# Kernel optimization log

Hardware: AMD Instinct MI355X
Metric: run time of the kernel (lower is better)

The kernel has to match this reference:

```python
import jax, jax.numpy as jnp
import numpy as np

FP8_MAX = 448.0  # e4m3fn max


def _fake_quant_fp8(x, scale):
    # quantize: scale, clamp, round-trip through float8_e4m3fn; dequantize by 1/scale
    xq = jnp.clip(x * scale, -FP8_MAX, FP8_MAX).astype(jnp.float8_e4m3fn)
    return xq.astype(jnp.float32) * (1.0 / scale)


def _compute_scale(x):
    amax = jnp.max(jnp.abs(x))
    return FP8_MAX / jnp.maximum(amax, 1e-12)


def setup_inputs() -> dict:
    key = jax.random.key(0)
    kx, kw = jax.random.split(key)
    x = jax.random.normal(kx, (8, 2048, 4096), dtype=jnp.float32)
    weight = jax.random.normal(kw, (4096, 4096), dtype=jnp.float32) * 0.02
    return {"x": x, "weight": weight}


def reference(x, weight):
    B, S, K = x.shape
    N = weight.shape[1]
    # weight path: per-tensor scale, fp8 round-trip (transpose in original is value-preserving)
    w_dq = _fake_quant_fp8(weight, _compute_scale(weight))  # [K, N]
    # activation path
    x2d = x.reshape(-1, K)  # [M, K]
    x_dq = _fake_quant_fp8(x2d, _compute_scale(x2d))
    out = x_dq @ w_dq  # fp32 GEMM, [M, N]
    return out.reshape(B, S, N)
```

## Files before the change

kernel.cpp:

```cpp
#include <hip/hip_runtime.h>
#include <stdint.h>

#define FP8_MAX 448.0f

typedef float f32x4 __attribute__((ext_vector_type(4)));
typedef int i32x8 __attribute__((ext_vector_type(8)));
typedef int i32x4 __attribute__((ext_vector_type(4)));

__device__ __forceinline__ unsigned int pack4_fp8(float4 v, float s) {
  float a = fminf(fmaxf(v.x * s, -FP8_MAX), FP8_MAX);
  float b = fminf(fmaxf(v.y * s, -FP8_MAX), FP8_MAX);
  float c = fminf(fmaxf(v.z * s, -FP8_MAX), FP8_MAX);
  float d = fminf(fmaxf(v.w * s, -FP8_MAX), FP8_MAX);
  unsigned int r = (unsigned int)__builtin_amdgcn_cvt_pk_fp8_f32(a, b, 0, false);
  r = (unsigned int)__builtin_amdgcn_cvt_pk_fp8_f32(c, d, (int)r, true);
  return r;
}

__device__ __forceinline__ void load16_to_lds(const void* g, void* l) {
  auto gp = (const __attribute__((address_space(1))) void*)(uintptr_t)g;
  auto lp = (__attribute__((address_space(3))) void*)(unsigned int)(uintptr_t)l;
  __builtin_amdgcn_global_load_lds(gp, lp, 16, 0, 0);
}

__global__ void amax_kernel(const float* __restrict__ p, int n4, unsigned int* __restrict__ slot) {
  int i = blockIdx.x * blockDim.x + threadIdx.x;
  int stride = gridDim.x * blockDim.x;
  float m = 0.0f;
  const float4* p4 = (const float4*)p;
  for (; i < n4; i += stride) {
    float4 v = p4[i];
    m = fmaxf(m, fmaxf(fmaxf(fabsf(v.x), fabsf(v.y)), fmaxf(fabsf(v.z), fabsf(v.w))));
  }
#pragma unroll
  for (int off = 32; off > 0; off >>= 1)
    m = fmaxf(m, __shfl_down(m, off, 64));
  __shared__ float wmax[4];
  int lane = threadIdx.x & 63;
  int wv = threadIdx.x >> 6;
  if (lane == 0) wmax[wv] = m;
  __syncthreads();
  if (threadIdx.x == 0) {
    m = fmaxf(fmaxf(wmax[0], wmax[1]), fmaxf(wmax[2], wmax[3]));
    atomicMax(slot, __float_as_uint(m));
  }
}

__global__ void quant_x_kernel(const float* __restrict__ x, unsigned int* __restrict__ xq,
                               const unsigned int* __restrict__ hdr, int n4) {
  float s = FP8_MAX / fmaxf(__uint_as_float(hdr[0]), 1e-12f);
  int i = blockIdx.x * blockDim.x + threadIdx.x;
  int stride = gridDim.x * blockDim.x;
  const float4* x4 = (const float4*)x;
  for (; i < n4; i += stride)
    xq[i] = pack4_fp8(x4[i], s);
}

__global__ void quant_w_t_kernel(const float* __restrict__ w, unsigned char* __restrict__ wqT,
                                 const unsigned int* __restrict__ hdr, int K, int N) {
  __shared__ unsigned int tileT[64][17];
  float s = FP8_MAX / fmaxf(__uint_as_float(hdr[1]), 1e-12f);
  int tk0 = blockIdx.y << 6;
  int tn0 = blockIdx.x << 6;
  int t = threadIdx.x;

  int rn = (t & 15) << 2;
  int rk = (t >> 4) << 2;
  unsigned int wrow[4];
#pragma unroll
  for (int j = 0; j < 4; ++j) {
    float4 v = *(const float4*)(w + (size_t)(tk0 + rk + j) * N + tn0 + rn);
    wrow[j] = pack4_fp8(v, s);
  }
#pragma unroll
  for (int i = 0; i < 4; ++i) {
    unsigned int colw = ((wrow[0] >> (8 * i)) & 0xffu)
                      | (((wrow[1] >> (8 * i)) & 0xffu) << 8)
                      | (((wrow[2] >> (8 * i)) & 0xffu) << 16)
                      | (((wrow[3] >> (8 * i)) & 0xffu) << 24);
    tileT[rn + i][rk >> 2] = colw;
  }
  __syncthreads();

  int n = t >> 2;
  int kc = (t & 3) << 2;
  uint4 v = make_uint4(tileT[n][kc], tileT[n][kc + 1], tileT[n][kc + 2], tileT[n][kc + 3]);
  *(uint4*)(wqT + (size_t)(tn0 + n) * K + tk0 + (kc << 2)) = v;
}

__global__ __launch_bounds__(256, 2) void gemm_fp8_kernel(
    const unsigned char* __restrict__ Aq,
    const unsigned char* __restrict__ Bq,
    const unsigned int* __restrict__ hdr,
    float* __restrict__ out, int M, int N, int K) {
  __shared__ __align__(16) unsigned char As[128 * 128];
  __shared__ __align__(16) unsigned char Bs[128 * 128];

  const int t = threadIdx.x;
  const int wave = t >> 6;
  const int lane = t & 63;
  const int row16 = lane & 15;
  const int quad = lane >> 4;
  const int m0 = blockIdx.y << 7;
  const int n0 = blockIdx.x << 7;
  const int waveM = (wave >> 1) << 6;
  const int waveN = (wave & 1) << 6;

  const int rowS = (wave << 3) + (lane >> 3);
  const int colS = (((lane & 7) ^ ((lane >> 3) & 7)) << 4);

  const unsigned char* ag = Aq + (size_t)(m0 + rowS) * K + colS;
  const unsigned char* bg = Bq + (size_t)(n0 + rowS) * K + colS;
  unsigned char* al = &As[rowS * 128 + ((lane & 7) << 4)];
  unsigned char* bl = &Bs[rowS * 128 + ((lane & 7) << 4)];
  const size_t gStep = (size_t)32 * K;

  const int sw = row16 & 7;
  const int off0 = (((quad << 1) ^ sw) << 4);

  f32x4 acc[4][4] = {};

  for (int k0 = 0; k0 < K; k0 += 128) {
#pragma unroll
    for (int j = 0; j < 4; ++j)
      load16_to_lds(ag + k0 + j * gStep, al + j * 4096);
#pragma unroll
    for (int j = 0; j < 4; ++j)
      load16_to_lds(bg + k0 + j * gStep, bl + j * 4096);
    __syncthreads();

    i32x8 af[4], bf[4];
#pragma unroll
    for (int mi = 0; mi < 4; ++mi) {
      const unsigned char* p = As + (waveM + mi * 16 + row16) * 128;
      i32x4 lo = *(const i32x4*)(p + off0);
      i32x4 hi = *(const i32x4*)(p + (off0 ^ 16));
      af[mi] = __builtin_shufflevector(lo, hi, 0, 1, 2, 3, 4, 5, 6, 7);
    }
#pragma unroll
    for (int ni = 0; ni < 4; ++ni) {
      const unsigned char* p = Bs + (waveN + ni * 16 + row16) * 128;
      i32x4 lo = *(const i32x4*)(p + off0);
      i32x4 hi = *(const i32x4*)(p + (off0 ^ 16));
      bf[ni] = __builtin_shufflevector(lo, hi, 0, 1, 2, 3, 4, 5, 6, 7);
    }
#pragma unroll
    for (int mi = 0; mi < 4; ++mi)
#pragma unroll
      for (int ni = 0; ni < 4; ++ni)
        acc[mi][ni] = __builtin_amdgcn_mfma_scale_f32_16x16x128_f8f6f4(
            af[mi], bf[ni], acc[mi][ni],
            0 , 0 ,
            0, 0x7f7f7f7f ,
            0, 0x7f7f7f7f );
    __syncthreads();
  }

  const float ax = fmaxf(__uint_as_float(hdr[0]), 1e-12f);
  const float aw = fmaxf(__uint_as_float(hdr[1]), 1e-12f);
  const float sc = (ax / FP8_MAX) * (aw / FP8_MAX);
#pragma unroll
  for (int mi = 0; mi < 4; ++mi) {
#pragma unroll
    for (int ni = 0; ni < 4; ++ni) {
      const int gc = n0 + waveN + ni * 16 + row16;
#pragma unroll
      for (int r = 0; r < 4; ++r) {
        const int gr = m0 + waveM + mi * 16 + quad * 4 + r;
        out[(size_t)gr * N + gc] = acc[mi][ni][r] * sc;
      }
    }
  }
}

extern "C" void kernel_launch(void* const* d_in, const int* in_sizes, int n_in,
                              void* d_out, int out_size, void* d_ws, size_t ws_size,
                              hipStream_t stream) {
  const float* x = (const float*)d_in[0];
  const float* w = (const float*)d_in[1];
  float* out = (float*)d_out;

  const int K = 4096;
  const int N = 4096;
  const int M = in_sizes[0] / K;

  unsigned int* hdr = (unsigned int*)d_ws;
  unsigned char* xq = (unsigned char*)d_ws + 16;
  unsigned char* wqT = xq + (size_t)M * K;

  hipMemsetAsync(d_ws, 0, 16, stream);

  amax_kernel<<<2048, 256, 0, stream>>>(x, (int)((size_t)M * K / 4), hdr + 0);
  amax_kernel<<<1024, 256, 0, stream>>>(w, (int)((size_t)K * N / 4), hdr + 1);

  quant_x_kernel<<<4096, 256, 0, stream>>>(x, (unsigned int*)xq, hdr, (int)((size_t)M * K / 4));
  quant_w_t_kernel<<<dim3(N / 64, K / 64), 256, 0, stream>>>(w, wqT, hdr, K, N);

  gemm_fp8_kernel<<<dim3(N / 128, M / 128), 256, 0, stream>>>(xq, wqT, hdr, out, M, N, K);
}
```

Baseline: 886.8 us.

## Use 256x256 double-buffered pipelined FP8 GEMM and fuse amax kernels

The FP8 GEMM moves from 128x128 tiles with 256 threads to 256x256 tiles with 512 threads and a 128 KB double-buffered LDS. Global-to-LDS loads for the next tiles are interleaved with MFMA quarters, using explicit vmcnt/lgkmcnt waits, barriers and s_setprio. The goal is to hide load latency and raise data reuse per block. The two amax reductions are also merged into a single launch. The costs are higher LDS use, which leaves one block per CU, and hand-placed waits that must stay correct as the pipeline runs down.

```diff
diff --git a/kernel.cpp b/kernel.cpp
--- a/kernel.cpp
+++ b/kernel.cpp
@@ -23,11 +23,20 @@
   __builtin_amdgcn_global_load_lds(gp, lp, 16, 0, 0);
 }
 
-__global__ void amax_kernel(const float* __restrict__ p, int n4, unsigned int* __restrict__ slot) {
-  int i = blockIdx.x * blockDim.x + threadIdx.x;
-  int stride = gridDim.x * blockDim.x;
+__global__ void amax2_kernel(const float* __restrict__ x, int n4x,
+                             const float* __restrict__ w, int n4w,
+                             unsigned int* __restrict__ hdr) {
+  const float4* p4;
+  int n4, base, nblk;
+  unsigned int* slot;
+  if (blockIdx.x < 2048) {
+    p4 = (const float4*)x; n4 = n4x; base = blockIdx.x; nblk = 2048; slot = hdr;
+  } else {
+    p4 = (const float4*)w; n4 = n4w; base = blockIdx.x - 2048; nblk = 512; slot = hdr + 1;
+  }
+  int i = base * blockDim.x + threadIdx.x;
+  int stride = nblk * blockDim.x;
   float m = 0.0f;
-  const float4* p4 = (const float4*)p;
   for (; i < n4; i += stride) {
     float4 v = p4[i];
     m = fmaxf(m, fmaxf(fmaxf(fabsf(v.x), fabsf(v.y)), fmaxf(fabsf(v.z), fabsf(v.w))));
@@ -88,85 +97,150 @@
   *(uint4*)(wqT + (size_t)(tn0 + n) * K + tk0 + (kc << 2)) = v;
 }
 
-__global__ __launch_bounds__(256, 2) void gemm_fp8_kernel(
+__device__ __forceinline__ i32x8 read_frag(const unsigned char* p, int off0) {
+  i32x4 lo = *(const i32x4*)(p + off0);
+  i32x4 hi = *(const i32x4*)(p + (off0 ^ 16));
+  return __builtin_shufflevector(lo, hi, 0, 1, 2, 3, 4, 5, 6, 7);
+}
+
+#define MFMA1(a, b, c) \
+  __builtin_amdgcn_mfma_scale_f32_16x16x128_f8f6f4(a, b, c, 0, 0, 0, 0x7f7f7f7f, 0, 0x7f7f7f7f)
+
+#define MFMA_Q(M0_, N0_)                                              \
+  do {                                                                \
+    __builtin_amdgcn_s_setprio(1);                                    \
+    acc[M0_ + 0][N0_ + 0] = MFMA1(af[0], bf[N0_ + 0], acc[M0_ + 0][N0_ + 0]); \
+    acc[M0_ + 0][N0_ + 1] = MFMA1(af[0], bf[N0_ + 1], acc[M0_ + 0][N0_ + 1]); \
+    acc[M0_ + 1][N0_ + 0] = MFMA1(af[1], bf[N0_ + 0], acc[M0_ + 1][N0_ + 0]); \
+    acc[M0_ + 1][N0_ + 1] = MFMA1(af[1], bf[N0_ + 1], acc[M0_ + 1][N0_ + 1]); \
+    acc[M0_ + 2][N0_ + 0] = MFMA1(af[2], bf[N0_ + 0], acc[M0_ + 2][N0_ + 0]); \
+    acc[M0_ + 2][N0_ + 1] = MFMA1(af[2], bf[N0_ + 1], acc[M0_ + 2][N0_ + 1]); \
+    acc[M0_ + 3][N0_ + 0] = MFMA1(af[3], bf[N0_ + 0], acc[M0_ + 3][N0_ + 0]); \
+    acc[M0_ + 3][N0_ + 1] = MFMA1(af[3], bf[N0_ + 1], acc[M0_ + 3][N0_ + 1]); \
+    __builtin_amdgcn_s_setprio(0);                                    \
+  } while (0)
+
+#define BAR() __builtin_amdgcn_s_barrier()
+#define LGKM0()                                           \
+  do {                                                    \
+    asm volatile("s_waitcnt lgkmcnt(0)" ::: "memory");    \
+    __builtin_amdgcn_sched_barrier(0);                    \
+  } while (0)
+#define VMCNT(N_)                                               \
+  do {                                                          \
+    asm volatile("s_waitcnt vmcnt(" #N_ ")" ::: "memory");      \
+    __builtin_amdgcn_sched_barrier(0);                          \
+  } while (0)
+
+__global__ __launch_bounds__(512, 2) void gemm_fp8_kernel(
     const unsigned char* __restrict__ Aq,
     const unsigned char* __restrict__ Bq,
     const unsigned int* __restrict__ hdr,
     float* __restrict__ out, int M, int N, int K) {
-  __shared__ __align__(16) unsigned char As[128 * 128];
-  __shared__ __align__(16) unsigned char Bs[128 * 128];
+  __shared__ __align__(16) unsigned char smem[131072];
 
   const int t = threadIdx.x;
   const int wave = t >> 6;
   const int lane = t & 63;
   const int row16 = lane & 15;
   const int quad = lane >> 4;
-  const int m0 = blockIdx.y << 7;
-  const int n0 = blockIdx.x << 7;
-  const int waveM = (wave >> 1) << 6;
-  const int waveN = (wave & 1) << 6;
-
-  const int rowS = (wave << 3) + (lane >> 3);
-  const int colS = (((lane & 7) ^ ((lane >> 3) & 7)) << 4);
-
-  const unsigned char* ag = Aq + (size_t)(m0 + rowS) * K + colS;
-  const unsigned char* bg = Bq + (size_t)(n0 + rowS) * K + colS;
-  unsigned char* al = &As[rowS * 128 + ((lane & 7) << 4)];
-  unsigned char* bl = &Bs[rowS * 128 + ((lane & 7) << 4)];
-  const size_t gStep = (size_t)32 * K;
-
-  const int sw = row16 & 7;
-  const int off0 = (((quad << 1) ^ sw) << 4);
-
-  f32x4 acc[4][4] = {};
-
-  for (int k0 = 0; k0 < K; k0 += 128) {
-#pragma unroll
-    for (int j = 0; j < 4; ++j)
-      load16_to_lds(ag + k0 + j * gStep, al + j * 4096);
-#pragma unroll
-    for (int j = 0; j < 4; ++j)
-      load16_to_lds(bg + k0 + j * gStep, bl + j * 4096);
-    __syncthreads();
-
+  const int wr = wave >> 2;
+  const int wc = wave & 3;
+  const int m0 = blockIdx.y << 8;
+  const int n0 = blockIdx.x << 8;
+
+  const int sRow = (wave << 3) + (lane >> 3);
+  const int sCol = (((lane & 7) ^ (lane >> 3)) << 4);
+  const unsigned char* agBase = Aq + (size_t)(m0 + sRow) * K + sCol;
+  const unsigned char* bgBase = Bq + (size_t)(n0 + sRow) * K + sCol;
+  const int ldsStageOff = (wave << 10) + (lane << 4);
+
+  auto stageA = [&](int u, int h) {
+    const int buf = (u & 1) << 15;
+#pragma unroll
+    for (int r = 0; r < 2; ++r)
+      load16_to_lds(agBase + (size_t)((h << 7) + (r << 6)) * K + ((size_t)u << 7),
+                    smem + buf + (h << 14) + (r << 13) + ldsStageOff);
+  };
+  auto stageB = [&](int u, int h) {
+    const int buf = (u & 1) << 15;
+#pragma unroll
+    for (int r = 0; r < 2; ++r)
+      load16_to_lds(bgBase + (size_t)((h << 7) + (r << 6)) * K + ((size_t)u << 7),
+                    smem + 65536 + buf + (h << 14) + (r << 13) + ldsStageOff);
+  };
+
+  const int off0 = (((quad << 1) ^ (row16 & 7)) << 4);
+  const int aRow = (wr << 7) + row16;
+  const int bRow = (wc << 6) + row16;
+
+  f32x4 acc[8][4] = {};
+
+  const int NT = K >> 7;
+
+  stageA(0, 0); stageA(0, 1); stageB(0, 0); stageB(0, 1);
+  stageA(1, 0); stageB(1, 0);
+  VMCNT(4);
+  BAR();
+
+  auto tile_body = [&](int tt, bool stg1, bool stg2, int waitN) {
+    const int buf = (tt & 1) << 15;
+    const unsigned char* Ab = smem + buf;
+    const unsigned char* Bb = smem + 65536 + buf;
     i32x8 af[4], bf[4];
-#pragma unroll
-    for (int mi = 0; mi < 4; ++mi) {
-      const unsigned char* p = As + (waveM + mi * 16 + row16) * 128;
-      i32x4 lo = *(const i32x4*)(p + off0);
-      i32x4 hi = *(const i32x4*)(p + (off0 ^ 16));
-      af[mi] = __builtin_shufflevector(lo, hi, 0, 1, 2, 3, 4, 5, 6, 7);
+    af[0] = read_frag(Ab + ((aRow + 0) << 7), off0);
+    af[1] = read_frag(Ab + ((aRow + 16) << 7), off0);
+    af[2] = read_frag(Ab + ((aRow + 32) << 7), off0);
+    af[3] = read_frag(Ab + ((aRow + 48) << 7), off0);
+    bf[0] = read_frag(Bb + ((bRow + 0) << 7), off0);
+    bf[1] = read_frag(Bb + ((bRow + 16) << 7), off0);
+    if (stg1) stageA(tt + 1, 1);
+    BAR();
+    LGKM0();
+    MFMA_Q(0, 0);
+    BAR();
+    bf[2] = read_frag(Bb + ((bRow + 32) << 7), off0);
+    bf[3] = read_frag(Bb + ((bRow + 48) << 7), off0);
+    if (stg1) stageB(tt + 1, 1);
+    BAR();
+    LGKM0();
+    MFMA_Q(0, 2);
+    BAR();
+    af[0] = read_frag(Ab + ((aRow + 64) << 7), off0);
+    af[1] = read_frag(Ab + ((aRow + 80) << 7), off0);
+    af[2] = read_frag(Ab + ((aRow + 96) << 7), off0);
+    af[3] = read_frag(Ab + ((aRow + 112) << 7), off0);
+    if (stg2) stageB(tt + 2, 0);
+    BAR();
+    LGKM0();
+    MFMA_Q(4, 0);
+    BAR();
+    if (stg2) stageA(tt + 2, 0);
+    if (waitN == 4) {
+      VMCNT(4);
+    } else if (waitN == 0) {
+      VMCNT(0);
     }
-#pragma unroll
-    for (int ni = 0; ni < 4; ++ni) {
-      const unsigned char* p = Bs + (waveN + ni * 16 + row16) * 128;
-      i32x4 lo = *(const i32x4*)(p + off0);
-      i32x4 hi = *(const i32x4*)(p + (off0 ^ 16));
-      bf[ni] = __builtin_shufflevector(lo, hi, 0, 1, 2, 3, 4, 5, 6, 7);
-    }
-#pragma unroll
-    for (int mi = 0; mi < 4; ++mi)
-#pragma unroll
-      for (int ni = 0; ni < 4; ++ni)
-        acc[mi][ni] = __builtin_amdgcn_mfma_scale_f32_16x16x128_f8f6f4(
-            af[mi], bf[ni], acc[mi][ni],
-            0 , 0 ,
-            0, 0x7f7f7f7f ,
-            0, 0x7f7f7f7f );
-    __syncthreads();
-  }
+    BAR();
+    MFMA_Q(4, 2);
+    BAR();
+  };
+
+  for (int tt = 0; tt < NT - 2; ++tt) tile_body(tt, true, true, 4);
+  tile_body(NT - 2, true, false, 0);
+  tile_body(NT - 1, false, false, -1);
 
   const float ax = fmaxf(__uint_as_float(hdr[0]), 1e-12f);
   const float aw = fmaxf(__uint_as_float(hdr[1]), 1e-12f);
   const float sc = (ax / FP8_MAX) * (aw / FP8_MAX);
 #pragma unroll
-  for (int mi = 0; mi < 4; ++mi) {
+  for (int mi = 0; mi < 8; ++mi) {
 #pragma unroll
     for (int ni = 0; ni < 4; ++ni) {
-      const int gc = n0 + waveN + ni * 16 + row16;
+      const int gc = n0 + (wc << 6) + ni * 16 + row16;
 #pragma unroll
       for (int r = 0; r < 4; ++r) {
-        const int gr = m0 + waveM + mi * 16 + quad * 4 + r;
+        const int gr = m0 + (wr << 7) + mi * 16 + quad * 4 + r;
         out[(size_t)gr * N + gc] = acc[mi][ni][r] * sc;
       }
     }
@@ -190,11 +264,11 @@
 
   hipMemsetAsync(d_ws, 0, 16, stream);
 
-  amax_kernel<<<2048, 256, 0, stream>>>(x, (int)((size_t)M * K / 4), hdr + 0);
-  amax_kernel<<<1024, 256, 0, stream>>>(w, (int)((size_t)K * N / 4), hdr + 1);
+  amax2_kernel<<<2560, 256, 0, stream>>>(x, (int)((size_t)M * K / 4), w,
+                                         (int)((size_t)K * N / 4), hdr);
 
   quant_x_kernel<<<4096, 256, 0, stream>>>(x, (unsigned int*)xq, hdr, (int)((size_t)M * K / 4));
   quant_w_t_kernel<<<dim3(N / 64, K / 64), 256, 0, stream>>>(w, wqT, hdr, K, N);
 
-  gemm_fp8_kernel<<<dim3(N / 128, M / 128), 256, 0, stream>>>(xq, wqT, hdr, out, M, N, K);
-}
+  gemm_fp8_kernel<<<dim3(N / 256, M / 256), 512, 0, stream>>>(xq, wqT, hdr, out, M, N, K);
+}
```

New measurement: 808.9 us. 1.1x faster.
